# Kernel tuning notes

Hardware: AMD Instinct MI355X
Metric: run time of the kernel (lower is better)

The kernel has to match this reference:

```python
import jax, jax.numpy as jnp
import numpy as np

N_NODES = 50000
N_EDGES = 800000
NODE_FEATURES = 128
HIDDEN = 64
N_CLASSES = 6


def gcn_conv(x, src, dst, W, b, n_nodes):
    """PyG GCNConv: out = D^{-1/2}(A+I)D^{-1/2} X W + b (self-loops included)."""
    deg = jax.ops.segment_sum(jnp.ones_like(dst, dtype=x.dtype), dst, num_segments=n_nodes)
    dinv = jnp.where(deg > 0, jax.lax.rsqrt(deg), 0.0)  # [N]
    h = x @ W  # [N, out] - transform before gather (fewer bytes moved)
    norm = dinv[src] * dinv[dst]  # [E+N]
    msg = h[src] * norm[:, None]  # [E+N, out]
    out = jax.ops.segment_sum(msg, dst, num_segments=n_nodes)  # [N, out]
    return out + b


def setup_inputs() -> dict:
    key = jax.random.key(0)
    ks = jax.random.split(key, 8)
    x = jax.random.normal(ks[0], (N_NODES, NODE_FEATURES), dtype=jnp.float32)
    edge_index = jax.random.randint(ks[1], (2, N_EDGES), 0, N_NODES, dtype=jnp.int64)
    W1 = jax.random.normal(ks[2], (NODE_FEATURES, HIDDEN), dtype=jnp.float32) * (1.0 / np.sqrt(NODE_FEATURES))
    b1 = jnp.zeros((HIDDEN,), dtype=jnp.float32)
    W2 = jax.random.normal(ks[3], (HIDDEN, HIDDEN), dtype=jnp.float32) * (1.0 / np.sqrt(HIDDEN))
    b2 = jnp.zeros((HIDDEN,), dtype=jnp.float32)
    Wc = jax.random.normal(ks[4], (HIDDEN * N_NODES, N_CLASSES), dtype=jnp.float32) * (1.0 / np.sqrt(HIDDEN * N_NODES))
    bc = jnp.zeros((N_CLASSES,), dtype=jnp.float32)
    return {"x": x, "edge_index": edge_index, "W1": W1, "b1": b1, "W2": W2, "b2": b2, "Wc": Wc, "bc": bc}


def reference(x, edge_index, W1, b1, W2, b2, Wc, bc):
    n_nodes = x.shape[0]
    loops = jnp.arange(n_nodes, dtype=edge_index.dtype)
    src = jnp.concatenate([edge_index[0], loops])
    dst = jnp.concatenate([edge_index[1], loops])
    h = jax.nn.relu(gcn_conv(x, src, dst, W1, b1, n_nodes))
    h = jax.nn.relu(gcn_conv(h, src, dst, W2, b2, n_nodes))
    logits = h.reshape(1, -1) @ Wc + bc  # [1, n_classes]
    return jax.nn.softmax(logits, axis=1)
```

## Files before the change

### kernel.cpp

```cpp
#include <hip/hip_runtime.h>
#include <math.h>


#define NCH 256
#define RBITS 10
#define NR_MAX 64

__device__ __forceinline__ ushort f32_to_bf16(float f) {
  unsigned u = __float_as_uint(f);
  return (ushort)((u + 0x7fffu + ((u >> 16) & 1u)) >> 16);
}
__device__ __forceinline__ float bf16_to_f32(ushort h) {
  return __uint_as_float(((unsigned)h) << 16);
}


__global__ __launch_bounds__(256) void hist_ranges(
    const int* __restrict__ dst, int* __restrict__ ghist, int NR, int E) {
  __shared__ int h[NR_MAX];
  int tid = threadIdx.x, c = blockIdx.x;
  if (tid < NR) h[tid] = 0;
  __syncthreads();
  int E4 = E >> 2;
  int CH4 = (E4 + NCH - 1) / NCH;
  int i0 = c * CH4, i1 = min(i0 + CH4, E4);
  const int4* d4 = (const int4*)dst;
  for (int i = i0 + tid; i < i1; i += 256) {
    int4 d = d4[i];
    atomicAdd(&h[d.x >> RBITS], 1);
    atomicAdd(&h[d.y >> RBITS], 1);
    atomicAdd(&h[d.z >> RBITS], 1);
    atomicAdd(&h[d.w >> RBITS], 1);
  }
  if (c == NCH - 1) {
    for (int e = (E4 << 2) + tid; e < E; e += 256) atomicAdd(&h[dst[e] >> RBITS], 1);
  }
  __syncthreads();
  if (tid < NR) ghist[tid * NCH + c] = h[tid];
}


__global__ __launch_bounds__(1024) void scan_ghist(int* __restrict__ g, int M) {
  __shared__ int wtot[16];
  int tid = threadIdx.x, lane = tid & 63, wv = tid >> 6;
  int SEG = (M + 1023) >> 10;
  int base = tid * SEG;
  int s = 0;
  for (int k = 0; k < SEG; ++k) { int i = base + k; if (i < M) s += g[i]; }
  int x = s;
#pragma unroll
  for (int d = 1; d < 64; d <<= 1) { int y = __shfl_up(x, d, 64); if (lane >= d) x += y; }
  if (lane == 63) wtot[wv] = x;
  __syncthreads();
  if (wv == 0 && lane < 16) {
    int t = wtot[lane], xx = t;
#pragma unroll
    for (int d = 1; d < 16; d <<= 1) { int y = __shfl_up(xx, d, 64); if (lane >= d) xx += y; }
    wtot[lane] = xx - t;
  }
  __syncthreads();
  int run = x - s + wtot[wv];
  for (int k = 0; k < SEG; ++k) {
    int i = base + k;
    if (i < M) { int tmp = g[i]; g[i] = run; run += tmp; }
  }
}


__global__ __launch_bounds__(256) void scatter_ranges(
    const int* __restrict__ src, const int* __restrict__ dst,
    const int* __restrict__ ghist, int2* __restrict__ ebuf, int NR, int E) {
  __shared__ int cur[NR_MAX];
  int tid = threadIdx.x, c = blockIdx.x;
  if (tid < NR) cur[tid] = ghist[tid * NCH + c];
  __syncthreads();
  int E4 = E >> 2;
  int CH4 = (E4 + NCH - 1) / NCH;
  int i0 = c * CH4, i1 = min(i0 + CH4, E4);
  const int4* d4 = (const int4*)dst;
  const int4* s4 = (const int4*)src;
  for (int i = i0 + tid; i < i1; i += 256) {
    int4 d = d4[i];
    int4 s = s4[i];
    ebuf[atomicAdd(&cur[d.x >> RBITS], 1)] = make_int2(s.x, d.x);
    ebuf[atomicAdd(&cur[d.y >> RBITS], 1)] = make_int2(s.y, d.y);
    ebuf[atomicAdd(&cur[d.z >> RBITS], 1)] = make_int2(s.z, d.z);
    ebuf[atomicAdd(&cur[d.w >> RBITS], 1)] = make_int2(s.w, d.w);
  }
  if (c == NCH - 1) {
    for (int e = (E4 << 2) + tid; e < E; e += 256)
      ebuf[atomicAdd(&cur[dst[e] >> RBITS], 1)] = make_int2(src[e], dst[e]);
  }
}


__global__ __launch_bounds__(1024) void csr_range(
    const int2* __restrict__ ebuf, const int* __restrict__ ghist,
    int* __restrict__ offs, int* __restrict__ srt, float* __restrict__ dinv,
    int N, int E, int NR) {
  __shared__ int hist[1024];
  __shared__ int wtot[16];
  int r = blockIdx.x;
  int lo = r << RBITS;
  int len = min(1024, N - lo);
  int tid = threadIdx.x, lane = tid & 63, wv = tid >> 6;
  int S  = ghist[r * NCH];
  int S1 = (r + 1 < NR) ? ghist[(r + 1) * NCH] : E;
  if (tid < len) hist[tid] = 0;
  __syncthreads();
  for (int i = S + tid; i < S1; i += 1024) atomicAdd(&hist[ebuf[i].y - lo], 1);
  __syncthreads();
  int v = (tid < len) ? hist[tid] : 0;
  if (tid < len) dinv[lo + tid] = rsqrtf((float)(v + 1));
  int x = v;
#pragma unroll
  for (int d = 1; d < 64; d <<= 1) { int y = __shfl_up(x, d, 64); if (lane >= d) x += y; }
  if (lane == 63) wtot[wv] = x;
  __syncthreads();
  if (wv == 0 && lane < 16) {
    int t = wtot[lane], xx = t;
#pragma unroll
    for (int d = 1; d < 16; d <<= 1) { int y = __shfl_up(xx, d, 64); if (lane >= d) xx += y; }
    wtot[lane] = xx - t;
  }
  __syncthreads();
  int excl = x - v + wtot[wv];
  if (tid < len) {
    offs[lo + tid] = S + excl;
    hist[tid] = S + excl;
  }
  if (r == 0 && tid == 0) offs[N] = E;
  __syncthreads();
  for (int i = S + tid; i < S1; i += 1024) {
    int2 e = ebuf[i];
    srt[atomicAdd(&hist[e.y - lo], 1)] = e.x;
  }
}


template <int K, int ROWS>
__global__ __launch_bounds__(256) void gemm_scale(
    const float* __restrict__ X, const float* __restrict__ W,
    const float* __restrict__ dinv, ushort* __restrict__ Gb, int N) {
  __shared__ float smw[K * 64];
  __shared__ float xs[ROWS * K];
  int tid = threadIdx.x, lane = tid & 63, wv = tid >> 6;
  for (int idx = tid; idx < K * 16; idx += 256)
    ((float4*)smw)[idx] = ((const float4*)W)[idx];
  int row0 = blockIdx.x * ROWS;
  int base = row0 * K;
  int cnt4 = (min(ROWS * K, N * K - base)) >> 2;
  const float4* X4 = (const float4*)(X + base);
  for (int idx = tid; idx < cnt4; idx += 256) ((float4*)xs)[idx] = X4[idx];
  __syncthreads();

  constexpr int RW = ROWS / 4;
  float acc[RW];
#pragma unroll
  for (int r = 0; r < RW; ++r) acc[r] = 0.f;
  const float* xr = &xs[(wv * RW) * K];
#pragma unroll 4
  for (int k = 0; k < K; ++k) {
    float wval = smw[k * 64 + lane];
#pragma unroll
    for (int r = 0; r < RW; ++r) acc[r] = fmaf(xr[r * K + k], wval, acc[r]);
  }
#pragma unroll
  for (int r = 0; r < RW; ++r) {
    int row = row0 + wv * RW + r;
    if (row < N) Gb[(size_t)row * 64 + lane] = f32_to_bf16(acc[r] * dinv[row]);
  }
}


template <int CLS>
__global__ __launch_bounds__(256) void aggregate(
    const ushort* __restrict__ Gb, const int* __restrict__ offs,
    const int* __restrict__ srt, const float* __restrict__ dinv,
    const float* __restrict__ bias, const float* __restrict__ Wc,
    float* __restrict__ H, float* __restrict__ part, int N) {
  int lane = threadIdx.x & 63, wv = threadIdx.x >> 6;
  int sub = lane >> 4, fl = lane & 15;
  int node = blockIdx.x * 4 + wv;
  const ushort4* G2 = (const ushort4*)Gb;

  if (CLS == 0 && node >= N) return;

  int e0 = 0, e1 = 0;
  if (node < N) { e0 = offs[node]; e1 = offs[node + 1]; }
  int deg = e1 - e0;

  float4 accA = make_float4(0.f, 0.f, 0.f, 0.f);
  float4 accB = make_float4(0.f, 0.f, 0.f, 0.f);
  if (sub == 0 && node < N) {
    ushort4 q = G2[(size_t)node * 16 + fl];
    accA.x = bf16_to_f32(q.x); accA.y = bf16_to_f32(q.y);
    accA.z = bf16_to_f32(q.z); accA.w = bf16_to_f32(q.w);
  }

  int pre = (deg > 0) ? srt[e0 + min(lane, deg - 1)] : 0;

  int dcap = min(deg, 64);
  int base = 0;
  for (; base + 7 < dcap; base += 8) {
    int sA = __shfl(pre, base + sub, 64);
    int sB = __shfl(pre, base + 4 + sub, 64);
    ushort4 qA = G2[(size_t)sA * 16 + fl];
    ushort4 qB = G2[(size_t)sB * 16 + fl];
    accA.x += bf16_to_f32(qA.x); accA.y += bf16_to_f32(qA.y);
    accA.z += bf16_to_f32(qA.z); accA.w += bf16_to_f32(qA.w);
    accB.x += bf16_to_f32(qB.x); accB.y += bf16_to_f32(qB.y);
    accB.z += bf16_to_f32(qB.z); accB.w += bf16_to_f32(qB.w);
  }
  for (; base + 3 < dcap; base += 4) {
    int s = __shfl(pre, base + sub, 64);
    ushort4 q = G2[(size_t)s * 16 + fl];
    accA.x += bf16_to_f32(q.x); accA.y += bf16_to_f32(q.y);
    accA.z += bf16_to_f32(q.z); accA.w += bf16_to_f32(q.w);
  }
  int e = e0 + base;
  for (; e + 3 < e1; e += 4) {
    int s = srt[e + sub];
    ushort4 q = G2[(size_t)s * 16 + fl];
    accA.x += bf16_to_f32(q.x); accA.y += bf16_to_f32(q.y);
    accA.z += bf16_to_f32(q.z); accA.w += bf16_to_f32(q.w);
  }
  int rem = e1 - e;
  if (sub < rem) {
    int s = srt[e + sub];
    ushort4 q = G2[(size_t)s * 16 + fl];
    accA.x += bf16_to_f32(q.x); accA.y += bf16_to_f32(q.y);
    accA.z += bf16_to_f32(q.z); accA.w += bf16_to_f32(q.w);
  }

  float4 acc;
  acc.x = accA.x + accB.x; acc.y = accA.y + accB.y;
  acc.z = accA.z + accB.z; acc.w = accA.w + accB.w;
#pragma unroll
  for (int m = 16; m < 64; m <<= 1) {
    acc.x += __shfl_xor(acc.x, m, 64);
    acc.y += __shfl_xor(acc.y, m, 64);
    acc.z += __shfl_xor(acc.z, m, 64);
    acc.w += __shfl_xor(acc.w, m, 64);
  }

  if (CLS == 0) {
    if (sub == 0 && node < N) {
      float dn = dinv[node];
      float4 bb = ((const float4*)bias)[fl];
      float4 r;
      r.x = fmaxf(fmaf(acc.x, dn, bb.x), 0.f);
      r.y = fmaxf(fmaf(acc.y, dn, bb.y), 0.f);
      r.z = fmaxf(fmaf(acc.z, dn, bb.z), 0.f);
      r.w = fmaxf(fmaf(acc.w, dn, bb.w), 0.f);
      ((float4*)H)[(size_t)node * 16 + fl] = r;
    }
  } else {
    float a[6] = {0.f, 0.f, 0.f, 0.f, 0.f, 0.f};
    if (sub == 0 && node < N) {
      float dn = dinv[node];
      float4 bb = ((const float4*)bias)[fl];
      float4 r;
      r.x = fmaxf(fmaf(acc.x, dn, bb.x), 0.f);
      r.y = fmaxf(fmaf(acc.y, dn, bb.y), 0.f);
      r.z = fmaxf(fmaf(acc.z, dn, bb.z), 0.f);
      r.w = fmaxf(fmaf(acc.w, dn, bb.w), 0.f);
      const float4* w4 = (const float4*)(Wc + (size_t)node * 384 + fl * 24);
      float4 w0 = w4[0], w1 = w4[1], w2 = w4[2], w3 = w4[3], w4_ = w4[4], w5 = w4[5];
      a[0] = fmaf(r.x, w0.x, fmaf(r.y, w1.z, fmaf(r.z, w3.x, r.w * w4_.z)));
      a[1] = fmaf(r.x, w0.y, fmaf(r.y, w1.w, fmaf(r.z, w3.y, r.w * w4_.w)));
      a[2] = fmaf(r.x, w0.z, fmaf(r.y, w2.x, fmaf(r.z, w3.z, r.w * w5.x)));
      a[3] = fmaf(r.x, w0.w, fmaf(r.y, w2.y, fmaf(r.z, w3.w, r.w * w5.y)));
      a[4] = fmaf(r.x, w1.x, fmaf(r.y, w2.z, fmaf(r.z, w4_.x, r.w * w5.z)));
      a[5] = fmaf(r.x, w1.y, fmaf(r.y, w2.w, fmaf(r.z, w4_.y, r.w * w5.w)));
    }
#pragma unroll
    for (int c = 0; c < 6; ++c) {
      for (int d = 32; d > 0; d >>= 1) a[c] += __shfl_down(a[c], d, 64);
    }
    __shared__ float sh[4][6];
    if (lane == 0) {
#pragma unroll
      for (int c = 0; c < 6; ++c) sh[wv][c] = a[c];
    }
    __syncthreads();
    if (threadIdx.x == 0) {
#pragma unroll
      for (int c = 0; c < 6; ++c)
        part[(size_t)blockIdx.x * 6 + c] = sh[0][c] + sh[1][c] + sh[2][c] + sh[3][c];
    }
  }
}

__global__ __launch_bounds__(1024) void reduce_softmax(
    const float* __restrict__ part, int nb,
    const float* __restrict__ bc, float* __restrict__ out) {
  int tid = threadIdx.x, lane = tid & 63, wv = tid >> 6;
  float a[6] = {0.f, 0.f, 0.f, 0.f, 0.f, 0.f};
  for (int b = tid; b < nb; b += 1024) {
    const float* p = part + (size_t)b * 6;
#pragma unroll
    for (int c = 0; c < 6; ++c) a[c] += p[c];
  }
#pragma unroll
  for (int c = 0; c < 6; ++c) {
    for (int d = 32; d > 0; d >>= 1) a[c] += __shfl_down(a[c], d, 64);
  }
  __shared__ float sh[16][6];
  if (lane == 0) {
#pragma unroll
    for (int c = 0; c < 6; ++c) sh[wv][c] = a[c];
  }
  __syncthreads();
  if (tid == 0) {
    float l[6], m = -1e30f;
#pragma unroll
    for (int c = 0; c < 6; ++c) {
      float t = 0.f;
      for (int w = 0; w < 16; ++w) t += sh[w][c];
      l[c] = t + bc[c];
      m = fmaxf(m, l[c]);
    }
    float s = 0.f;
#pragma unroll
    for (int c = 0; c < 6; ++c) { l[c] = __expf(l[c] - m); s += l[c]; }
    float inv = 1.f / s;
#pragma unroll
    for (int c = 0; c < 6; ++c) out[c] = l[c] * inv;
  }
}


static inline size_t align4up(size_t x) { return (x + 3) & ~(size_t)3; }

extern "C" void kernel_launch(void* const* d_in, const int* in_sizes, int n_in,
                              void* d_out, int out_size, void* d_ws, size_t ws_size,
                              hipStream_t stream) {
  const float* x  = (const float*)d_in[0];
  const int*   ei = (const int*)d_in[1];
  const float* W1 = (const float*)d_in[2];
  const float* b1 = (const float*)d_in[3];
  const float* W2 = (const float*)d_in[4];
  const float* b2 = (const float*)d_in[5];
  const float* Wc = (const float*)d_in[6];
  const float* bc = (const float*)d_in[7];
  float* out = (float*)d_out;

  const int N = in_sizes[0] / 128;
  const int E = in_sizes[1] / 2;
  const int* esrc = ei;
  const int* edst = ei + E;
  const int NR = (N + 1023) >> RBITS;
  const int AGRID = (N + 3) / 4;

  size_t o = 0;
  int* offs   = (int*)d_ws + o;           o = align4up(o + N + 1);
  int* srt    = (int*)d_ws + o;           o = align4up(o + E);
  float* dinv = (float*)d_ws + o;         o = align4up(o + N);
  int* ghist  = (int*)d_ws + o;           o = align4up(o + (size_t)NR * NCH);
  ushort* Gb  = (ushort*)((int*)d_ws + o); o = align4up(o + (size_t)N * 32);
  float* bufB = (float*)d_ws + o;         o = align4up(o + (size_t)N * 64);
  float* part = (float*)d_ws + o;         o = align4up(o + (size_t)AGRID * 6);
  int2* ebuf  = (int2*)bufB;

  hist_ranges<<<NCH, 256, 0, stream>>>(edst, ghist, NR, E);
  scan_ghist<<<1, 1024, 0, stream>>>(ghist, NR * NCH);
  scatter_ranges<<<NCH, 256, 0, stream>>>(esrc, edst, ghist, ebuf, NR, E);
  csr_range<<<NR, 1024, 0, stream>>>(ebuf, ghist, offs, srt, dinv, N, E, NR);

  gemm_scale<128, 32><<<(N + 31) / 32, 256, 0, stream>>>(x, W1, dinv, Gb, N);
  aggregate<0><<<AGRID, 256, 0, stream>>>(Gb, offs, srt, dinv, b1, nullptr, bufB, nullptr, N);
  gemm_scale<64, 32><<<(N + 31) / 32, 256, 0, stream>>>(bufB, W2, dinv, Gb, N);
  aggregate<1><<<AGRID, 256, 0, stream>>>(Gb, offs, srt, dinv, b2, Wc, nullptr, part, N);

  reduce_softmax<<<1, 1024, 0, stream>>>(part, AGRID, bc, out);
}
```

Baseline: 164.3 us.

## Split aggregation by source half for cache locality, fold ghist scan into consumers

```diff
diff --git a/kernel.cpp b/kernel.cpp
--- a/kernel.cpp
+++ b/kernel.cpp
@@ -6,12 +6,31 @@
 #define RBITS 10
 #define NR_MAX 64
 
+typedef float  f32x4 __attribute__((ext_vector_type(4)));
+typedef unsigned short u16x4 __attribute__((ext_vector_type(4)));
+
 __device__ __forceinline__ ushort f32_to_bf16(float f) {
   unsigned u = __float_as_uint(f);
   return (ushort)((u + 0x7fffu + ((u >> 16) & 1u)) >> 16);
 }
 __device__ __forceinline__ float bf16_to_f32(ushort h) {
   return __uint_as_float(((unsigned)h) << 16);
+}
+__device__ __forceinline__ float4 nt_ld_f4(const float* p) {
+  f32x4 v = __builtin_nontemporal_load((const f32x4*)p);
+  return make_float4(v.x, v.y, v.z, v.w);
+}
+__device__ __forceinline__ void nt_st_f4(float* p, float4 a) {
+  f32x4 v; v.x = a.x; v.y = a.y; v.z = a.z; v.w = a.w;
+  __builtin_nontemporal_store(v, (f32x4*)p);
+}
+__device__ __forceinline__ ushort4 nt_ld_u4(const ushort* p) {
+  u16x4 v = __builtin_nontemporal_load((const u16x4*)p);
+  ushort4 r; r.x = v.x; r.y = v.y; r.z = v.z; r.w = v.w;
+  return r;
+}
+__device__ __forceinline__ int nt_ld_i(const int* p) {
+  return __builtin_nontemporal_load(p);
 }
 
 
@@ -40,39 +59,33 @@
 }
 
 
-__global__ __launch_bounds__(1024) void scan_ghist(int* __restrict__ g, int M) {
-  __shared__ int wtot[16];
-  int tid = threadIdx.x, lane = tid & 63, wv = tid >> 6;
-  int SEG = (M + 1023) >> 10;
-  int base = tid * SEG;
-  int s = 0;
-  for (int k = 0; k < SEG; ++k) { int i = base + k; if (i < M) s += g[i]; }
-  int x = s;
-#pragma unroll
-  for (int d = 1; d < 64; d <<= 1) { int y = __shfl_up(x, d, 64); if (lane >= d) x += y; }
-  if (lane == 63) wtot[wv] = x;
-  __syncthreads();
-  if (wv == 0 && lane < 16) {
-    int t = wtot[lane], xx = t;
-#pragma unroll
-    for (int d = 1; d < 16; d <<= 1) { int y = __shfl_up(xx, d, 64); if (lane >= d) xx += y; }
-    wtot[lane] = xx - t;
-  }
-  __syncthreads();
-  int run = x - s + wtot[wv];
-  for (int k = 0; k < SEG; ++k) {
-    int i = base + k;
-    if (i < M) { int tmp = g[i]; g[i] = run; run += tmp; }
-  }
-}
-
-
 __global__ __launch_bounds__(256) void scatter_ranges(
     const int* __restrict__ src, const int* __restrict__ dst,
     const int* __restrict__ ghist, int2* __restrict__ ebuf, int NR, int E) {
   __shared__ int cur[NR_MAX];
+  __shared__ int rowpre[NR_MAX + 1];
   int tid = threadIdx.x, c = blockIdx.x;
-  if (tid < NR) cur[tid] = ghist[tid * NCH + c];
+  if (tid < NR) {
+    const int4* row = (const int4*)(ghist + tid * NCH);
+    int s = 0;
+    for (int q = 0; q < NCH / 4; ++q) { int4 v = row[q]; s += v.x + v.y + v.z + v.w; }
+    rowpre[tid + 1] = s;
+  }
+  __syncthreads();
+  if (tid == 0) {
+    rowpre[0] = 0;
+    for (int i = 1; i <= NR; ++i) rowpre[i] += rowpre[i - 1];
+  }
+  __syncthreads();
+  if (tid < NR) {
+    int s = rowpre[tid];
+    const int* row = ghist + tid * NCH;
+    const int4* row4 = (const int4*)row;
+    int c4 = c >> 2;
+    for (int q = 0; q < c4; ++q) { int4 v = row4[q]; s += v.x + v.y + v.z + v.w; }
+    for (int cc = c4 << 2; cc < c; ++cc) s += row[cc];
+    cur[tid] = s;
+  }
   __syncthreads();
   int E4 = E >> 2;
   int CH4 = (E4 + NCH - 1) / NCH;
@@ -96,21 +109,37 @@
 
 __global__ __launch_bounds__(1024) void csr_range(
     const int2* __restrict__ ebuf, const int* __restrict__ ghist,
-    int* __restrict__ offs, int* __restrict__ srt, float* __restrict__ dinv,
-    int N, int E, int NR) {
-  __shared__ int hist[1024];
+    int* __restrict__ offs, int* __restrict__ splits, int* __restrict__ srt,
+    float* __restrict__ dinv, int N, int E, int NR, int NHALF) {
+  __shared__ int hT[1024];
+  __shared__ int hL[1024];
   __shared__ int wtot[16];
+  __shared__ int rowpre[NR_MAX + 1];
   int r = blockIdx.x;
   int lo = r << RBITS;
   int len = min(1024, N - lo);
   int tid = threadIdx.x, lane = tid & 63, wv = tid >> 6;
-  int S  = ghist[r * NCH];
-  int S1 = (r + 1 < NR) ? ghist[(r + 1) * NCH] : E;
-  if (tid < len) hist[tid] = 0;
-  __syncthreads();
-  for (int i = S + tid; i < S1; i += 1024) atomicAdd(&hist[ebuf[i].y - lo], 1);
-  __syncthreads();
-  int v = (tid < len) ? hist[tid] : 0;
+  if (tid < NR) {
+    const int4* row = (const int4*)(ghist + tid * NCH);
+    int s = 0;
+    for (int q = 0; q < NCH / 4; ++q) { int4 v = row[q]; s += v.x + v.y + v.z + v.w; }
+    rowpre[tid + 1] = s;
+  }
+  if (tid < len) { hT[tid] = 0; hL[tid] = 0; }
+  __syncthreads();
+  if (tid == 0) {
+    rowpre[0] = 0;
+    for (int i = 1; i <= NR; ++i) rowpre[i] += rowpre[i - 1];
+  }
+  __syncthreads();
+  int S = rowpre[r], S1 = rowpre[r + 1];
+  for (int i = S + tid; i < S1; i += 1024) {
+    int2 e = ebuf[i];
+    atomicAdd(&hT[e.y - lo], 1);
+    if (e.x < NHALF) atomicAdd(&hL[e.y - lo], 1);
+  }
+  __syncthreads();
+  int v = (tid < len) ? hT[tid] : 0;
   if (tid < len) dinv[lo + tid] = rsqrtf((float)(v + 1));
   int x = v;
 #pragma unroll
@@ -126,14 +155,20 @@
   __syncthreads();
   int excl = x - v + wtot[wv];
   if (tid < len) {
-    offs[lo + tid] = S + excl;
-    hist[tid] = S + excl;
+    int base = S + excl;
+    int sp = base + hL[tid];
+    offs[lo + tid] = base;
+    splits[lo + tid] = sp;
+    hT[tid] = base;
+    hL[tid] = sp;
   }
   if (r == 0 && tid == 0) offs[N] = E;
   __syncthreads();
   for (int i = S + tid; i < S1; i += 1024) {
     int2 e = ebuf[i];
-    srt[atomicAdd(&hist[e.y - lo], 1)] = e.x;
+    int idx = e.y - lo;
+    int p = (e.x < NHALF) ? atomicAdd(&hT[idx], 1) : atomicAdd(&hL[idx], 1);
+    srt[p] = e.x;
   }
 }
 
@@ -173,32 +208,40 @@
 }
 
 
-template <int CLS>
+template <int PHASE, int CLS>
 __global__ __launch_bounds__(256) void aggregate(
     const ushort* __restrict__ Gb, const int* __restrict__ offs,
-    const int* __restrict__ srt, const float* __restrict__ dinv,
-    const float* __restrict__ bias, const float* __restrict__ Wc,
-    float* __restrict__ H, float* __restrict__ part, int N) {
+    const int* __restrict__ splits, const int* __restrict__ srt,
+    const float* __restrict__ dinv, const float* __restrict__ bias,
+    const float* __restrict__ Wc, float* __restrict__ H,
+    float* __restrict__ part, int N) {
   int lane = threadIdx.x & 63, wv = threadIdx.x >> 6;
   int sub = lane >> 4, fl = lane & 15;
   int node = blockIdx.x * 4 + wv;
   const ushort4* G2 = (const ushort4*)Gb;
 
-  if (CLS == 0 && node >= N) return;
+  if (!(PHASE == 1 && CLS == 1) && node >= N) return;
 
   int e0 = 0, e1 = 0;
-  if (node < N) { e0 = offs[node]; e1 = offs[node + 1]; }
+  if (node < N) {
+    if (PHASE == 0) { e0 = nt_ld_i(&offs[node]); e1 = nt_ld_i(&splits[node]); }
+    else            { e0 = nt_ld_i(&splits[node]); e1 = nt_ld_i(&offs[node + 1]); }
+  }
   int deg = e1 - e0;
 
   float4 accA = make_float4(0.f, 0.f, 0.f, 0.f);
   float4 accB = make_float4(0.f, 0.f, 0.f, 0.f);
   if (sub == 0 && node < N) {
-    ushort4 q = G2[(size_t)node * 16 + fl];
-    accA.x = bf16_to_f32(q.x); accA.y = bf16_to_f32(q.y);
-    accA.z = bf16_to_f32(q.z); accA.w = bf16_to_f32(q.w);
-  }
-
-  int pre = (deg > 0) ? srt[e0 + min(lane, deg - 1)] : 0;
+    if (PHASE == 0) {
+      ushort4 q = nt_ld_u4(&Gb[((size_t)node * 16 + fl) * 4]);
+      accA.x = bf16_to_f32(q.x); accA.y = bf16_to_f32(q.y);
+      accA.z = bf16_to_f32(q.z); accA.w = bf16_to_f32(q.w);
+    } else {
+      accA = nt_ld_f4(&H[((size_t)node * 16 + fl) * 4]);
+    }
+  }
+
+  int pre = (deg > 0) ? nt_ld_i(&srt[e0 + min(lane, deg - 1)]) : 0;
 
   int dcap = min(deg, 64);
   int base = 0;
@@ -220,14 +263,14 @@
   }
   int e = e0 + base;
   for (; e + 3 < e1; e += 4) {
-    int s = srt[e + sub];
+    int s = nt_ld_i(&srt[e + sub]);
     ushort4 q = G2[(size_t)s * 16 + fl];
     accA.x += bf16_to_f32(q.x); accA.y += bf16_to_f32(q.y);
     accA.z += bf16_to_f32(q.z); accA.w += bf16_to_f32(q.w);
   }
   int rem = e1 - e;
   if (sub < rem) {
-    int s = srt[e + sub];
+    int s = nt_ld_i(&srt[e + sub]);
     ushort4 q = G2[(size_t)s * 16 + fl];
     accA.x += bf16_to_f32(q.x); accA.y += bf16_to_f32(q.y);
     accA.z += bf16_to_f32(q.z); accA.w += bf16_to_f32(q.w);
@@ -244,7 +287,10 @@
     acc.w += __shfl_xor(acc.w, m, 64);
   }
 
-  if (CLS == 0) {
+  if (PHASE == 0) {
+    if (sub == 0 && node < N)
+      nt_st_f4(&H[((size_t)node * 16 + fl) * 4], acc);
+  } else if (CLS == 0) {
     if (sub == 0 && node < N) {
       float dn = dinv[node];
       float4 bb = ((const float4*)bias)[fl];
@@ -253,7 +299,7 @@
       r.y = fmaxf(fmaf(acc.y, dn, bb.y), 0.f);
       r.z = fmaxf(fmaf(acc.z, dn, bb.z), 0.f);
       r.w = fmaxf(fmaf(acc.w, dn, bb.w), 0.f);
-      ((float4*)H)[(size_t)node * 16 + fl] = r;
+      nt_st_f4(&H[((size_t)node * 16 + fl) * 4], r);
     }
   } else {
     float a[6] = {0.f, 0.f, 0.f, 0.f, 0.f, 0.f};
@@ -265,8 +311,9 @@
       r.y = fmaxf(fmaf(acc.y, dn, bb.y), 0.f);
       r.z = fmaxf(fmaf(acc.z, dn, bb.z), 0.f);
       r.w = fmaxf(fmaf(acc.w, dn, bb.w), 0.f);
-      const float4* w4 = (const float4*)(Wc + (size_t)node * 384 + fl * 24);
-      float4 w0 = w4[0], w1 = w4[1], w2 = w4[2], w3 = w4[3], w4_ = w4[4], w5 = w4[5];
+      const float* wp = Wc + (size_t)node * 384 + fl * 24;
+      float4 w0 = nt_ld_f4(wp), w1 = nt_ld_f4(wp + 4), w2 = nt_ld_f4(wp + 8);
+      float4 w3 = nt_ld_f4(wp + 12), w4_ = nt_ld_f4(wp + 16), w5 = nt_ld_f4(wp + 20);
       a[0] = fmaf(r.x, w0.x, fmaf(r.y, w1.z, fmaf(r.z, w3.x, r.w * w4_.z)));
       a[1] = fmaf(r.x, w0.y, fmaf(r.y, w1.w, fmaf(r.z, w3.y, r.w * w4_.w)));
       a[2] = fmaf(r.x, w0.z, fmaf(r.y, w2.x, fmaf(r.z, w3.z, r.w * w5.x)));
@@ -352,9 +399,11 @@
   const int* edst = ei + E;
   const int NR = (N + 1023) >> RBITS;
   const int AGRID = (N + 3) / 4;
+  const int NHALF = N / 2;
 
   size_t o = 0;
   int* offs   = (int*)d_ws + o;           o = align4up(o + N + 1);
+  int* splits = (int*)d_ws + o;           o = align4up(o + N);
   int* srt    = (int*)d_ws + o;           o = align4up(o + E);
   float* dinv = (float*)d_ws + o;         o = align4up(o + N);
   int* ghist  = (int*)d_ws + o;           o = align4up(o + (size_t)NR * NCH);
@@ -364,14 +413,15 @@
   int2* ebuf  = (int2*)bufB;
 
   hist_ranges<<<NCH, 256, 0, stream>>>(edst, ghist, NR, E);
-  scan_ghist<<<1, 1024, 0, stream>>>(ghist, NR * NCH);
   scatter_ranges<<<NCH, 256, 0, stream>>>(esrc, edst, ghist, ebuf, NR, E);
-  csr_range<<<NR, 1024, 0, stream>>>(ebuf, ghist, offs, srt, dinv, N, E, NR);
+  csr_range<<<NR, 1024, 0, stream>>>(ebuf, ghist, offs, splits, srt, dinv, N, E, NR, NHALF);
 
   gemm_scale<128, 32><<<(N + 31) / 32, 256, 0, stream>>>(x, W1, dinv, Gb, N);
-  aggregate<0><<<AGRID, 256, 0, stream>>>(Gb, offs, srt, dinv, b1, nullptr, bufB, nullptr, N);
+  aggregate<0, 0><<<AGRID, 256, 0, stream>>>(Gb, offs, splits, srt, dinv, b1, nullptr, bufB, nullptr, N);
+  aggregate<1, 0><<<AGRID, 256, 0, stream>>>(Gb, offs, splits, srt, dinv, b1, nullptr, bufB, nullptr, N);
   gemm_scale<64, 32><<<(N + 31) / 32, 256, 0, stream>>>(bufB, W2, dinv, Gb, N);
-  aggregate<1><<<AGRID, 256, 0, stream>>>(Gb, offs, srt, dinv, b2, Wc, nullptr, part, N);
+  aggregate<0, 0><<<AGRID, 256, 0, stream>>>(Gb, offs, splits, srt, dinv, b2, nullptr, bufB, nullptr, N);
+  aggregate<1, 1><<<AGRID, 256, 0, stream>>>(Gb, offs, splits, srt, dinv, b2, Wc, bufB, part, N);
 
   reduce_softmax<<<1, 1024, 0, stream>>>(part, AGRID, bc, out);
 }
```

Result: slower. 223.5 us (+36.0%).

## Fold ghist scan into consumers and process four nodes per wave in aggregate

Applied to the files above, without the earlier changes.

```diff
diff --git a/kernel.cpp b/kernel.cpp
--- a/kernel.cpp
+++ b/kernel.cpp
@@ -40,39 +40,33 @@
 }
 
 
-__global__ __launch_bounds__(1024) void scan_ghist(int* __restrict__ g, int M) {
-  __shared__ int wtot[16];
-  int tid = threadIdx.x, lane = tid & 63, wv = tid >> 6;
-  int SEG = (M + 1023) >> 10;
-  int base = tid * SEG;
-  int s = 0;
-  for (int k = 0; k < SEG; ++k) { int i = base + k; if (i < M) s += g[i]; }
-  int x = s;
-#pragma unroll
-  for (int d = 1; d < 64; d <<= 1) { int y = __shfl_up(x, d, 64); if (lane >= d) x += y; }
-  if (lane == 63) wtot[wv] = x;
-  __syncthreads();
-  if (wv == 0 && lane < 16) {
-    int t = wtot[lane], xx = t;
-#pragma unroll
-    for (int d = 1; d < 16; d <<= 1) { int y = __shfl_up(xx, d, 64); if (lane >= d) xx += y; }
-    wtot[lane] = xx - t;
-  }
-  __syncthreads();
-  int run = x - s + wtot[wv];
-  for (int k = 0; k < SEG; ++k) {
-    int i = base + k;
-    if (i < M) { int tmp = g[i]; g[i] = run; run += tmp; }
-  }
-}
-
-
 __global__ __launch_bounds__(256) void scatter_ranges(
     const int* __restrict__ src, const int* __restrict__ dst,
     const int* __restrict__ ghist, int2* __restrict__ ebuf, int NR, int E) {
   __shared__ int cur[NR_MAX];
+  __shared__ int rowpre[NR_MAX + 1];
   int tid = threadIdx.x, c = blockIdx.x;
-  if (tid < NR) cur[tid] = ghist[tid * NCH + c];
+  if (tid < NR) {
+    const int4* row = (const int4*)(ghist + tid * NCH);
+    int s = 0;
+    for (int q = 0; q < NCH / 4; ++q) { int4 v = row[q]; s += v.x + v.y + v.z + v.w; }
+    rowpre[tid + 1] = s;
+  }
+  __syncthreads();
+  if (tid == 0) {
+    rowpre[0] = 0;
+    for (int i = 1; i <= NR; ++i) rowpre[i] += rowpre[i - 1];
+  }
+  __syncthreads();
+  if (tid < NR) {
+    int s = rowpre[tid];
+    const int* row = ghist + tid * NCH;
+    const int4* row4 = (const int4*)row;
+    int c4 = c >> 2;
+    for (int q = 0; q < c4; ++q) { int4 v = row4[q]; s += v.x + v.y + v.z + v.w; }
+    for (int cc = c4 << 2; cc < c; ++cc) s += row[cc];
+    cur[tid] = s;
+  }
   __syncthreads();
   int E4 = E >> 2;
   int CH4 = (E4 + NCH - 1) / NCH;
@@ -100,14 +94,25 @@
     int N, int E, int NR) {
   __shared__ int hist[1024];
   __shared__ int wtot[16];
+  __shared__ int rowpre[NR_MAX + 1];
   int r = blockIdx.x;
   int lo = r << RBITS;
   int len = min(1024, N - lo);
   int tid = threadIdx.x, lane = tid & 63, wv = tid >> 6;
-  int S  = ghist[r * NCH];
-  int S1 = (r + 1 < NR) ? ghist[(r + 1) * NCH] : E;
+  if (tid < NR) {
+    const int4* row = (const int4*)(ghist + tid * NCH);
+    int s = 0;
+    for (int q = 0; q < NCH / 4; ++q) { int4 v = row[q]; s += v.x + v.y + v.z + v.w; }
+    rowpre[tid + 1] = s;
+  }
   if (tid < len) hist[tid] = 0;
   __syncthreads();
+  if (tid == 0) {
+    rowpre[0] = 0;
+    for (int i = 1; i <= NR; ++i) rowpre[i] += rowpre[i - 1];
+  }
+  __syncthreads();
+  int S = rowpre[r], S1 = rowpre[r + 1];
   for (int i = S + tid; i < S1; i += 1024) atomicAdd(&hist[ebuf[i].y - lo], 1);
   __syncthreads();
   int v = (tid < len) ? hist[tid] : 0;
@@ -173,6 +178,14 @@
 }
 
 
+#define AGG_GATHER(PRE, B, ACC)                                            \
+  {                                                                        \
+    int s_ = __shfl(PRE, (B) + sub, 64);                                   \
+    ushort4 q_ = G2[(size_t)s_ * 16 + fl];                                 \
+    ACC.x += bf16_to_f32(q_.x); ACC.y += bf16_to_f32(q_.y);                \
+    ACC.z += bf16_to_f32(q_.z); ACC.w += bf16_to_f32(q_.w);                \
+  }
+
 template <int CLS>
 __global__ __launch_bounds__(256) void aggregate(
     const ushort* __restrict__ Gb, const int* __restrict__ offs,
@@ -181,98 +194,152 @@
     float* __restrict__ H, float* __restrict__ part, int N) {
   int lane = threadIdx.x & 63, wv = threadIdx.x >> 6;
   int sub = lane >> 4, fl = lane & 15;
-  int node = blockIdx.x * 4 + wv;
+  int nb0 = (blockIdx.x * 4 + wv) * 4;
   const ushort4* G2 = (const ushort4*)Gb;
 
-  if (CLS == 0 && node >= N) return;
-
-  int e0 = 0, e1 = 0;
-  if (node < N) { e0 = offs[node]; e1 = offs[node + 1]; }
-  int deg = e1 - e0;
-
-  float4 accA = make_float4(0.f, 0.f, 0.f, 0.f);
-  float4 accB = make_float4(0.f, 0.f, 0.f, 0.f);
-  if (sub == 0 && node < N) {
-    ushort4 q = G2[(size_t)node * 16 + fl];
-    accA.x = bf16_to_f32(q.x); accA.y = bf16_to_f32(q.y);
-    accA.z = bf16_to_f32(q.z); accA.w = bf16_to_f32(q.w);
-  }
-
-  int pre = (deg > 0) ? srt[e0 + min(lane, deg - 1)] : 0;
-
-  int dcap = min(deg, 64);
-  int base = 0;
-  for (; base + 7 < dcap; base += 8) {
-    int sA = __shfl(pre, base + sub, 64);
-    int sB = __shfl(pre, base + 4 + sub, 64);
-    ushort4 qA = G2[(size_t)sA * 16 + fl];
-    ushort4 qB = G2[(size_t)sB * 16 + fl];
-    accA.x += bf16_to_f32(qA.x); accA.y += bf16_to_f32(qA.y);
-    accA.z += bf16_to_f32(qA.z); accA.w += bf16_to_f32(qA.w);
-    accB.x += bf16_to_f32(qB.x); accB.y += bf16_to_f32(qB.y);
-    accB.z += bf16_to_f32(qB.z); accB.w += bf16_to_f32(qB.w);
-  }
-  for (; base + 3 < dcap; base += 4) {
-    int s = __shfl(pre, base + sub, 64);
-    ushort4 q = G2[(size_t)s * 16 + fl];
-    accA.x += bf16_to_f32(q.x); accA.y += bf16_to_f32(q.y);
-    accA.z += bf16_to_f32(q.z); accA.w += bf16_to_f32(q.w);
-  }
-  int e = e0 + base;
-  for (; e + 3 < e1; e += 4) {
-    int s = srt[e + sub];
-    ushort4 q = G2[(size_t)s * 16 + fl];
-    accA.x += bf16_to_f32(q.x); accA.y += bf16_to_f32(q.y);
-    accA.z += bf16_to_f32(q.z); accA.w += bf16_to_f32(q.w);
-  }
-  int rem = e1 - e;
-  if (sub < rem) {
-    int s = srt[e + sub];
-    ushort4 q = G2[(size_t)s * 16 + fl];
-    accA.x += bf16_to_f32(q.x); accA.y += bf16_to_f32(q.y);
-    accA.z += bf16_to_f32(q.z); accA.w += bf16_to_f32(q.w);
-  }
-
-  float4 acc;
-  acc.x = accA.x + accB.x; acc.y = accA.y + accB.y;
-  acc.z = accA.z + accB.z; acc.w = accA.w + accB.w;
+  int o_l = 0;
+  if (lane < 5) o_l = offs[min(nb0 + lane, N)];
+  int e00 = __shfl(o_l, 0, 64), e01 = __shfl(o_l, 1, 64);
+  int e02 = __shfl(o_l, 2, 64), e03 = __shfl(o_l, 3, 64);
+  int e04 = __shfl(o_l, 4, 64);
+  bool v0 = nb0 < N, v1 = nb0 + 1 < N, v2 = nb0 + 2 < N, v3 = nb0 + 3 < N;
+  int d0 = v0 ? e01 - e00 : 0, d1 = v1 ? e02 - e01 : 0;
+  int d2 = v2 ? e03 - e02 : 0, d3 = v3 ? e04 - e03 : 0;
+
+  int pre0 = 0, pre1 = 0, pre2 = 0, pre3 = 0;
+  if (d0 > 0) pre0 = srt[e00 + min(lane, d0 - 1)];
+  if (d1 > 0) pre1 = srt[e01 + min(lane, d1 - 1)];
+  if (d2 > 0) pre2 = srt[e02 + min(lane, d2 - 1)];
+  if (d3 > 0) pre3 = srt[e03 + min(lane, d3 - 1)];
+
+  float4 acc0 = make_float4(0.f, 0.f, 0.f, 0.f), acc1 = acc0, acc2 = acc0, acc3 = acc0;
+  if (sub == 0) {
+    if (v0) { ushort4 q = G2[(size_t)(nb0    ) * 16 + fl];
+      acc0.x = bf16_to_f32(q.x); acc0.y = bf16_to_f32(q.y);
+      acc0.z = bf16_to_f32(q.z); acc0.w = bf16_to_f32(q.w); }
+    if (v1) { ushort4 q = G2[(size_t)(nb0 + 1) * 16 + fl];
+      acc1.x = bf16_to_f32(q.x); acc1.y = bf16_to_f32(q.y);
+      acc1.z = bf16_to_f32(q.z); acc1.w = bf16_to_f32(q.w); }
+    if (v2) { ushort4 q = G2[(size_t)(nb0 + 2) * 16 + fl];
+      acc2.x = bf16_to_f32(q.x); acc2.y = bf16_to_f32(q.y);
+      acc2.z = bf16_to_f32(q.z); acc2.w = bf16_to_f32(q.w); }
+    if (v3) { ushort4 q = G2[(size_t)(nb0 + 3) * 16 + fl];
+      acc3.x = bf16_to_f32(q.x); acc3.y = bf16_to_f32(q.y);
+      acc3.z = bf16_to_f32(q.z); acc3.w = bf16_to_f32(q.w); }
+  }
+
+  int dc0 = min(d0, 64), dc1 = min(d1, 64), dc2 = min(d2, 64), dc3 = min(d3, 64);
+  int Rmax = max(max(dc0, dc1), max(dc2, dc3)) >> 2;
+  for (int r = 0; r < Rmax; ++r) {
+    int b = r << 2;
+    if (b + 4 <= dc0) AGG_GATHER(pre0, b, acc0);
+    if (b + 4 <= dc1) AGG_GATHER(pre1, b, acc1);
+    if (b + 4 <= dc2) AGG_GATHER(pre2, b, acc2);
+    if (b + 4 <= dc3) AGG_GATHER(pre3, b, acc3);
+  }
+  { int t = dc0 & ~3, rem = dc0 - t;
+    if (rem) { int s = __shfl(pre0, t + sub, 64);
+      if (sub < rem) { ushort4 q = G2[(size_t)s * 16 + fl];
+        acc0.x += bf16_to_f32(q.x); acc0.y += bf16_to_f32(q.y);
+        acc0.z += bf16_to_f32(q.z); acc0.w += bf16_to_f32(q.w); } } }
+  { int t = dc1 & ~3, rem = dc1 - t;
+    if (rem) { int s = __shfl(pre1, t + sub, 64);
+      if (sub < rem) { ushort4 q = G2[(size_t)s * 16 + fl];
+        acc1.x += bf16_to_f32(q.x); acc1.y += bf16_to_f32(q.y);
+        acc1.z += bf16_to_f32(q.z); acc1.w += bf16_to_f32(q.w); } } }
+  { int t = dc2 & ~3, rem = dc2 - t;
+    if (rem) { int s = __shfl(pre2, t + sub, 64);
+      if (sub < rem) { ushort4 q = G2[(size_t)s * 16 + fl];
+        acc2.x += bf16_to_f32(q.x); acc2.y += bf16_to_f32(q.y);
+        acc2.z += bf16_to_f32(q.z); acc2.w += bf16_to_f32(q.w); } } }
+  { int t = dc3 & ~3, rem = dc3 - t;
+    if (rem) { int s = __shfl(pre3, t + sub, 64);
+      if (sub < rem) { ushort4 q = G2[(size_t)s * 16 + fl];
+        acc3.x += bf16_to_f32(q.x); acc3.y += bf16_to_f32(q.y);
+        acc3.z += bf16_to_f32(q.z); acc3.w += bf16_to_f32(q.w); } } }
+
+  if (d0 > 64) { for (int e = e00 + 64; e < e01; ++e) { if (sub == 0) {
+        int s = srt[e]; ushort4 q = G2[(size_t)s * 16 + fl];
+        acc0.x += bf16_to_f32(q.x); acc0.y += bf16_to_f32(q.y);
+        acc0.z += bf16_to_f32(q.z); acc0.w += bf16_to_f32(q.w); } } }
+  if (d1 > 64) { for (int e = e01 + 64; e < e02; ++e) { if (sub == 0) {
+        int s = srt[e]; ushort4 q = G2[(size_t)s * 16 + fl];
+        acc1.x += bf16_to_f32(q.x); acc1.y += bf16_to_f32(q.y);
+        acc1.z += bf16_to_f32(q.z); acc1.w += bf16_to_f32(q.w); } } }
+  if (d2 > 64) { for (int e = e02 + 64; e < e03; ++e) { if (sub == 0) {
+        int s = srt[e]; ushort4 q = G2[(size_t)s * 16 + fl];
+        acc2.x += bf16_to_f32(q.x); acc2.y += bf16_to_f32(q.y);
+        acc2.z += bf16_to_f32(q.z); acc2.w += bf16_to_f32(q.w); } } }
+  if (d3 > 64) { for (int e = e03 + 64; e < e04; ++e) { if (sub == 0) {
+        int s = srt[e]; ushort4 q = G2[(size_t)s * 16 + fl];
+        acc3.x += bf16_to_f32(q.x); acc3.y += bf16_to_f32(q.y);
+        acc3.z += bf16_to_f32(q.z); acc3.w += bf16_to_f32(q.w); } } }
+
 #pragma unroll
   for (int m = 16; m < 64; m <<= 1) {
-    acc.x += __shfl_xor(acc.x, m, 64);
-    acc.y += __shfl_xor(acc.y, m, 64);
-    acc.z += __shfl_xor(acc.z, m, 64);
-    acc.w += __shfl_xor(acc.w, m, 64);
+    acc0.x += __shfl_xor(acc0.x, m, 64); acc0.y += __shfl_xor(acc0.y, m, 64);
+    acc0.z += __shfl_xor(acc0.z, m, 64); acc0.w += __shfl_xor(acc0.w, m, 64);
+    acc1.x += __shfl_xor(acc1.x, m, 64); acc1.y += __shfl_xor(acc1.y, m, 64);
+    acc1.z += __shfl_xor(acc1.z, m, 64); acc1.w += __shfl_xor(acc1.w, m, 64);
+    acc2.x += __shfl_xor(acc2.x, m, 64); acc2.y += __shfl_xor(acc2.y, m, 64);
+    acc2.z += __shfl_xor(acc2.z, m, 64); acc2.w += __shfl_xor(acc2.w, m, 64);
+    acc3.x += __shfl_xor(acc3.x, m, 64); acc3.y += __shfl_xor(acc3.y, m, 64);
+    acc3.z += __shfl_xor(acc3.z, m, 64); acc3.w += __shfl_xor(acc3.w, m, 64);
   }
 
   if (CLS == 0) {
-    if (sub == 0 && node < N) {
-      float dn = dinv[node];
+    if (sub == 0) {
       float4 bb = ((const float4*)bias)[fl];
-      float4 r;
-      r.x = fmaxf(fmaf(acc.x, dn, bb.x), 0.f);
-      r.y = fmaxf(fmaf(acc.y, dn, bb.y), 0.f);
-      r.z = fmaxf(fmaf(acc.z, dn, bb.z), 0.f);
-      r.w = fmaxf(fmaf(acc.w, dn, bb.w), 0.f);
-      ((float4*)H)[(size_t)node * 16 + fl] = r;
+      if (v0) { float dn = dinv[nb0];
+        float4 r; r.x = fmaxf(fmaf(acc0.x, dn, bb.x), 0.f);
+        r.y = fmaxf(fmaf(acc0.y, dn, bb.y), 0.f);
+        r.z = fmaxf(fmaf(acc0.z, dn, bb.z), 0.f);
+        r.w = fmaxf(fmaf(acc0.w, dn, bb.w), 0.f);
+        ((float4*)H)[(size_t)(nb0    ) * 16 + fl] = r; }
+      if (v1) { float dn = dinv[nb0 + 1];
+        float4 r; r.x = fmaxf(fmaf(acc1.x, dn, bb.x), 0.f);
+        r.y = fmaxf(fmaf(acc1.y, dn, bb.y), 0.f);
+        r.z = fmaxf(fmaf(acc1.z, dn, bb.z), 0.f);
+        r.w = fmaxf(fmaf(acc1.w, dn, bb.w), 0.f);
+        ((float4*)H)[(size_t)(nb0 + 1) * 16 + fl] = r; }
+      if (v2) { float dn = dinv[nb0 + 2];
+        float4 r; r.x = fmaxf(fmaf(acc2.x, dn, bb.x), 0.f);
+        r.y = fmaxf(fmaf(acc2.y, dn, bb.y), 0.f);
+        r.z = fmaxf(fmaf(acc2.z, dn, bb.z), 0.f);
+        r.w = fmaxf(fmaf(acc2.w, dn, bb.w), 0.f);
+        ((float4*)H)[(size_t)(nb0 + 2) * 16 + fl] = r; }
+      if (v3) { float dn = dinv[nb0 + 3];
+        float4 r; r.x = fmaxf(fmaf(acc3.x, dn, bb.x), 0.f);
+        r.y = fmaxf(fmaf(acc3.y, dn, bb.y), 0.f);
+        r.z = fmaxf(fmaf(acc3.z, dn, bb.z), 0.f);
+        r.w = fmaxf(fmaf(acc3.w, dn, bb.w), 0.f);
+        ((float4*)H)[(size_t)(nb0 + 3) * 16 + fl] = r; }
     }
   } else {
     float a[6] = {0.f, 0.f, 0.f, 0.f, 0.f, 0.f};
-    if (sub == 0 && node < N) {
-      float dn = dinv[node];
+    if (sub == 0) {
       float4 bb = ((const float4*)bias)[fl];
-      float4 r;
-      r.x = fmaxf(fmaf(acc.x, dn, bb.x), 0.f);
-      r.y = fmaxf(fmaf(acc.y, dn, bb.y), 0.f);
-      r.z = fmaxf(fmaf(acc.z, dn, bb.z), 0.f);
-      r.w = fmaxf(fmaf(acc.w, dn, bb.w), 0.f);
-      const float4* w4 = (const float4*)(Wc + (size_t)node * 384 + fl * 24);
-      float4 w0 = w4[0], w1 = w4[1], w2 = w4[2], w3 = w4[3], w4_ = w4[4], w5 = w4[5];
-      a[0] = fmaf(r.x, w0.x, fmaf(r.y, w1.z, fmaf(r.z, w3.x, r.w * w4_.z)));
-      a[1] = fmaf(r.x, w0.y, fmaf(r.y, w1.w, fmaf(r.z, w3.y, r.w * w4_.w)));
-      a[2] = fmaf(r.x, w0.z, fmaf(r.y, w2.x, fmaf(r.z, w3.z, r.w * w5.x)));
-      a[3] = fmaf(r.x, w0.w, fmaf(r.y, w2.y, fmaf(r.z, w3.w, r.w * w5.y)));
-      a[4] = fmaf(r.x, w1.x, fmaf(r.y, w2.z, fmaf(r.z, w4_.x, r.w * w5.z)));
-      a[5] = fmaf(r.x, w1.y, fmaf(r.y, w2.w, fmaf(r.z, w4_.y, r.w * w5.w)));
+#pragma unroll
+      for (int i = 0; i < 4; ++i) {
+        bool vi = (i == 0) ? v0 : (i == 1) ? v1 : (i == 2) ? v2 : v3;
+        if (!vi) continue;
+        float4 ac = (i == 0) ? acc0 : (i == 1) ? acc1 : (i == 2) ? acc2 : acc3;
+        int node = nb0 + i;
+        float dn = dinv[node];
+        float4 r;
+        r.x = fmaxf(fmaf(ac.x, dn, bb.x), 0.f);
+        r.y = fmaxf(fmaf(ac.y, dn, bb.y), 0.f);
+        r.z = fmaxf(fmaf(ac.z, dn, bb.z), 0.f);
+        r.w = fmaxf(fmaf(ac.w, dn, bb.w), 0.f);
+        const float4* w4 = (const float4*)(Wc + (size_t)node * 384 + fl * 24);
+        float4 w0 = w4[0], w1 = w4[1], w2 = w4[2], w3 = w4[3], w4_ = w4[4], w5 = w4[5];
+        a[0] += fmaf(r.x, w0.x, fmaf(r.y, w1.z, fmaf(r.z, w3.x, r.w * w4_.z)));
+        a[1] += fmaf(r.x, w0.y, fmaf(r.y, w1.w, fmaf(r.z, w3.y, r.w * w4_.w)));
+        a[2] += fmaf(r.x, w0.z, fmaf(r.y, w2.x, fmaf(r.z, w3.z, r.w * w5.x)));
+        a[3] += fmaf(r.x, w0.w, fmaf(r.y, w2.y, fmaf(r.z, w3.w, r.w * w5.y)));
+        a[4] += fmaf(r.x, w1.x, fmaf(r.y, w2.z, fmaf(r.z, w4_.x, r.w * w5.z)));
+        a[5] += fmaf(r.x, w1.y, fmaf(r.y, w2.w, fmaf(r.z, w4_.y, r.w * w5.w)));
+      }
     }
 #pragma unroll
     for (int c = 0; c < 6; ++c) {
@@ -351,7 +418,7 @@
   const int* esrc = ei;
   const int* edst = ei + E;
   const int NR = (N + 1023) >> RBITS;
-  const int AGRID = (N + 3) / 4;
+  const int AGRID = (N + 15) / 16;
 
   size_t o = 0;
   int* offs   = (int*)d_ws + o;           o = align4up(o + N + 1);
@@ -364,7 +431,6 @@
   int2* ebuf  = (int2*)bufB;
 
   hist_ranges<<<NCH, 256, 0, stream>>>(edst, ghist, NR, E);
-  scan_ghist<<<1, 1024, 0, stream>>>(ghist, NR * NCH);
   scatter_ranges<<<NCH, 256, 0, stream>>>(esrc, edst, ghist, ebuf, NR, E);
   csr_range<<<NR, 1024, 0, stream>>>(ebuf, ghist, offs, srt, dinv, N, E, NR);
 
```

Result: no change. 165.1 us (+0.5%).

## Fuse layer-2 GEMM into layer-1 aggregation and drop the scan kernel

Applied to the files above, without the earlier changes.

```diff
diff --git a/kernel.cpp b/kernel.cpp
--- a/kernel.cpp
+++ b/kernel.cpp
@@ -40,39 +40,33 @@
 }
 
 
-__global__ __launch_bounds__(1024) void scan_ghist(int* __restrict__ g, int M) {
-  __shared__ int wtot[16];
-  int tid = threadIdx.x, lane = tid & 63, wv = tid >> 6;
-  int SEG = (M + 1023) >> 10;
-  int base = tid * SEG;
-  int s = 0;
-  for (int k = 0; k < SEG; ++k) { int i = base + k; if (i < M) s += g[i]; }
-  int x = s;
-#pragma unroll
-  for (int d = 1; d < 64; d <<= 1) { int y = __shfl_up(x, d, 64); if (lane >= d) x += y; }
-  if (lane == 63) wtot[wv] = x;
-  __syncthreads();
-  if (wv == 0 && lane < 16) {
-    int t = wtot[lane], xx = t;
-#pragma unroll
-    for (int d = 1; d < 16; d <<= 1) { int y = __shfl_up(xx, d, 64); if (lane >= d) xx += y; }
-    wtot[lane] = xx - t;
-  }
-  __syncthreads();
-  int run = x - s + wtot[wv];
-  for (int k = 0; k < SEG; ++k) {
-    int i = base + k;
-    if (i < M) { int tmp = g[i]; g[i] = run; run += tmp; }
-  }
-}
-
-
 __global__ __launch_bounds__(256) void scatter_ranges(
     const int* __restrict__ src, const int* __restrict__ dst,
     const int* __restrict__ ghist, int2* __restrict__ ebuf, int NR, int E) {
   __shared__ int cur[NR_MAX];
+  __shared__ int rowpre[NR_MAX + 1];
   int tid = threadIdx.x, c = blockIdx.x;
-  if (tid < NR) cur[tid] = ghist[tid * NCH + c];
+  if (tid < NR) {
+    const int4* row = (const int4*)(ghist + tid * NCH);
+    int s = 0;
+    for (int q = 0; q < NCH / 4; ++q) { int4 v = row[q]; s += v.x + v.y + v.z + v.w; }
+    rowpre[tid + 1] = s;
+  }
+  __syncthreads();
+  if (tid == 0) {
+    rowpre[0] = 0;
+    for (int i = 1; i <= NR; ++i) rowpre[i] += rowpre[i - 1];
+  }
+  __syncthreads();
+  if (tid < NR) {
+    int s = rowpre[tid];
+    const int* row = ghist + tid * NCH;
+    const int4* row4 = (const int4*)row;
+    int c4 = c >> 2;
+    for (int q = 0; q < c4; ++q) { int4 v = row4[q]; s += v.x + v.y + v.z + v.w; }
+    for (int cc = c4 << 2; cc < c; ++cc) s += row[cc];
+    cur[tid] = s;
+  }
   __syncthreads();
   int E4 = E >> 2;
   int CH4 = (E4 + NCH - 1) / NCH;
@@ -100,14 +94,25 @@
     int N, int E, int NR) {
   __shared__ int hist[1024];
   __shared__ int wtot[16];
+  __shared__ int rowpre[NR_MAX + 1];
   int r = blockIdx.x;
   int lo = r << RBITS;
   int len = min(1024, N - lo);
   int tid = threadIdx.x, lane = tid & 63, wv = tid >> 6;
-  int S  = ghist[r * NCH];
-  int S1 = (r + 1 < NR) ? ghist[(r + 1) * NCH] : E;
+  if (tid < NR) {
+    const int4* row = (const int4*)(ghist + tid * NCH);
+    int s = 0;
+    for (int q = 0; q < NCH / 4; ++q) { int4 v = row[q]; s += v.x + v.y + v.z + v.w; }
+    rowpre[tid + 1] = s;
+  }
   if (tid < len) hist[tid] = 0;
   __syncthreads();
+  if (tid == 0) {
+    rowpre[0] = 0;
+    for (int i = 1; i <= NR; ++i) rowpre[i] += rowpre[i - 1];
+  }
+  __syncthreads();
+  int S = rowpre[r], S1 = rowpre[r + 1];
   for (int i = S + tid; i < S1; i += 1024) atomicAdd(&hist[ebuf[i].y - lo], 1);
   __syncthreads();
   int v = (tid < len) ? hist[tid] : 0;
@@ -173,18 +178,18 @@
 }
 
 
-template <int CLS>
+template <int MODE>
 __global__ __launch_bounds__(256) void aggregate(
     const ushort* __restrict__ Gb, const int* __restrict__ offs,
     const int* __restrict__ srt, const float* __restrict__ dinv,
-    const float* __restrict__ bias, const float* __restrict__ Wc,
-    float* __restrict__ H, float* __restrict__ part, int N) {
+    const float* __restrict__ bias, const float* __restrict__ Wx,
+    ushort* __restrict__ Gout, float* __restrict__ part, int N) {
   int lane = threadIdx.x & 63, wv = threadIdx.x >> 6;
   int sub = lane >> 4, fl = lane & 15;
   int node = blockIdx.x * 4 + wv;
   const ushort4* G2 = (const ushort4*)Gb;
 
-  if (CLS == 0 && node >= N) return;
+  if (MODE == 0 && node >= N) return;
 
   int e0 = 0, e1 = 0;
   if (node < N) { e0 = offs[node]; e1 = offs[node + 1]; }
@@ -244,8 +249,8 @@
     acc.w += __shfl_xor(acc.w, m, 64);
   }
 
-  if (CLS == 0) {
-    if (sub == 0 && node < N) {
+  if (MODE == 0) {
+    if (node < N) {
       float dn = dinv[node];
       float4 bb = ((const float4*)bias)[fl];
       float4 r;
@@ -253,7 +258,40 @@
       r.y = fmaxf(fmaf(acc.y, dn, bb.y), 0.f);
       r.z = fmaxf(fmaf(acc.z, dn, bb.z), 0.f);
       r.w = fmaxf(fmaf(acc.w, dn, bb.w), 0.f);
-      ((float4*)H)[(size_t)node * 16 + fl] = r;
+      float4 o = make_float4(0.f, 0.f, 0.f, 0.f);
+#pragma unroll
+      for (int t = 0; t < 4; ++t) {
+        int g = 4 * sub + t;
+        int srcl = (lane & 48) | g;
+        float h0 = __shfl(r.x, srcl, 64);
+        float h1 = __shfl(r.y, srcl, 64);
+        float h2 = __shfl(r.z, srcl, 64);
+        float h3 = __shfl(r.w, srcl, 64);
+        const float* wp = Wx + (size_t)(4 * g) * 64 + 4 * fl;
+        float4 w0 = *(const float4*)(wp);
+        float4 w1 = *(const float4*)(wp + 64);
+        float4 w2 = *(const float4*)(wp + 128);
+        float4 w3 = *(const float4*)(wp + 192);
+        o.x = fmaf(h0, w0.x, fmaf(h1, w1.x, fmaf(h2, w2.x, fmaf(h3, w3.x, o.x))));
+        o.y = fmaf(h0, w0.y, fmaf(h1, w1.y, fmaf(h2, w2.y, fmaf(h3, w3.y, o.y))));
+        o.z = fmaf(h0, w0.z, fmaf(h1, w1.z, fmaf(h2, w2.z, fmaf(h3, w3.z, o.z))));
+        o.w = fmaf(h0, w0.w, fmaf(h1, w1.w, fmaf(h2, w2.w, fmaf(h3, w3.w, o.w))));
+      }
+#pragma unroll
+      for (int m = 16; m < 64; m <<= 1) {
+        o.x += __shfl_xor(o.x, m, 64);
+        o.y += __shfl_xor(o.y, m, 64);
+        o.z += __shfl_xor(o.z, m, 64);
+        o.w += __shfl_xor(o.w, m, 64);
+      }
+      if (sub == 0) {
+        ushort4 q;
+        q.x = f32_to_bf16(o.x * dn);
+        q.y = f32_to_bf16(o.y * dn);
+        q.z = f32_to_bf16(o.z * dn);
+        q.w = f32_to_bf16(o.w * dn);
+        ((ushort4*)Gout)[(size_t)node * 16 + fl] = q;
+      }
     }
   } else {
     float a[6] = {0.f, 0.f, 0.f, 0.f, 0.f, 0.f};
@@ -265,7 +303,7 @@
       r.y = fmaxf(fmaf(acc.y, dn, bb.y), 0.f);
       r.z = fmaxf(fmaf(acc.z, dn, bb.z), 0.f);
       r.w = fmaxf(fmaf(acc.w, dn, bb.w), 0.f);
-      const float4* w4 = (const float4*)(Wc + (size_t)node * 384 + fl * 24);
+      const float4* w4 = (const float4*)(Wx + (size_t)node * 384 + fl * 24);
       float4 w0 = w4[0], w1 = w4[1], w2 = w4[2], w3 = w4[3], w4_ = w4[4], w5 = w4[5];
       a[0] = fmaf(r.x, w0.x, fmaf(r.y, w1.z, fmaf(r.z, w3.x, r.w * w4_.z)));
       a[1] = fmaf(r.x, w0.y, fmaf(r.y, w1.w, fmaf(r.z, w3.y, r.w * w4_.w)));
@@ -354,24 +392,22 @@
   const int AGRID = (N + 3) / 4;
 
   size_t o = 0;
-  int* offs   = (int*)d_ws + o;           o = align4up(o + N + 1);
-  int* srt    = (int*)d_ws + o;           o = align4up(o + E);
-  float* dinv = (float*)d_ws + o;         o = align4up(o + N);
-  int* ghist  = (int*)d_ws + o;           o = align4up(o + (size_t)NR * NCH);
-  ushort* Gb  = (ushort*)((int*)d_ws + o); o = align4up(o + (size_t)N * 32);
-  float* bufB = (float*)d_ws + o;         o = align4up(o + (size_t)N * 64);
-  float* part = (float*)d_ws + o;         o = align4up(o + (size_t)AGRID * 6);
-  int2* ebuf  = (int2*)bufB;
+  int* offs   = (int*)d_ws + o;            o = align4up(o + N + 1);
+  int* srt    = (int*)d_ws + o;            o = align4up(o + E);
+  float* dinv = (float*)d_ws + o;          o = align4up(o + N);
+  int* ghist  = (int*)d_ws + o;            o = align4up(o + (size_t)NR * NCH);
+  ushort* Gb1 = (ushort*)((int*)d_ws + o); o = align4up(o + (size_t)N * 32);
+  ushort* Gb2 = (ushort*)((int*)d_ws + o); o = align4up(o + max((size_t)N * 32, (size_t)E * 2));
+  float* part = (float*)d_ws + o;          o = align4up(o + (size_t)AGRID * 6);
+  int2* ebuf  = (int2*)Gb2;
 
   hist_ranges<<<NCH, 256, 0, stream>>>(edst, ghist, NR, E);
-  scan_ghist<<<1, 1024, 0, stream>>>(ghist, NR * NCH);
   scatter_ranges<<<NCH, 256, 0, stream>>>(esrc, edst, ghist, ebuf, NR, E);
   csr_range<<<NR, 1024, 0, stream>>>(ebuf, ghist, offs, srt, dinv, N, E, NR);
 
-  gemm_scale<128, 32><<<(N + 31) / 32, 256, 0, stream>>>(x, W1, dinv, Gb, N);
-  aggregate<0><<<AGRID, 256, 0, stream>>>(Gb, offs, srt, dinv, b1, nullptr, bufB, nullptr, N);
-  gemm_scale<64, 32><<<(N + 31) / 32, 256, 0, stream>>>(bufB, W2, dinv, Gb, N);
-  aggregate<1><<<AGRID, 256, 0, stream>>>(Gb, offs, srt, dinv, b2, Wc, nullptr, part, N);
+  gemm_scale<128, 32><<<(N + 31) / 32, 256, 0, stream>>>(x, W1, dinv, Gb1, N);
+  aggregate<0><<<AGRID, 256, 0, stream>>>(Gb1, offs, srt, dinv, b1, W2, Gb2, nullptr, N);
+  aggregate<1><<<AGRID, 256, 0, stream>>>(Gb2, offs, srt, dinv, b2, Wc, nullptr, part, N);
 
   reduce_softmax<<<1, 1024, 0, stream>>>(part, AGRID, bc, out);
 }
```

Result: faster. 159.7 us (-2.8%).
